# Performance work log

Hardware: AMD Instinct MI355X
Metric: run time of the kernel (lower is better)

Reference implementation:

```python
import jax, jax.numpy as jnp
import numpy as np

DIM = 512  # module's self.dim, used for the softmax scale (note: NOT head dim)

def setup_inputs() -> dict:
    key = jax.random.key(0)
    kq, kk, kv = jax.random.split(key, 3)
    shape = (4, 8, 2048, 64)  # [B, H, S, Dh]
    q = jax.random.normal(kq, shape, dtype=jnp.float32)
    k = jax.random.normal(kk, shape, dtype=jnp.float32)
    v = jax.random.normal(kv, shape, dtype=jnp.float32)
    return {"q": q, "k": k, "v": v, "n": 2048}

def reference(q, k, v, n):
    # scores = q @ k^T, then divide by sqrt(dim) AFTER matmul (as in source)
    scores = jnp.einsum('bhqd,bhkd->bhqk', q, k)
    scale = jnp.sqrt(jnp.asarray(DIM, dtype=scores.dtype))
    p_attn = jax.nn.softmax(scores / scale, axis=-1)
    return jnp.einsum('bhqk,bhkd->bhqd', p_attn, v)
```

## Files before the change

kernel.cpp:

```cpp
#include <hip/hip_runtime.h>


using half8   = __attribute__((ext_vector_type(8))) _Float16;
using half4   = __attribute__((ext_vector_type(4))) _Float16;
using half2v  = __attribute__((ext_vector_type(2))) _Float16;
using f32x4   = __attribute__((ext_vector_type(4))) float;
using f32x16  = __attribute__((ext_vector_type(16))) float;
using int4v   = __attribute__((ext_vector_type(4))) int;
using ushort8 = __attribute__((ext_vector_type(8))) unsigned short;

static __device__ __forceinline__ half2v cvt_pk(float a, float b) {
    return __builtin_bit_cast(half2v, __builtin_amdgcn_cvt_pkrtz(a, b));
}
static __device__ __forceinline__ int cvt_pk_i(float a, float b) {
    return __builtin_bit_cast(int, __builtin_amdgcn_cvt_pkrtz(a, b));
}

#define SEQ   2048
#define DH    64
#define QB    128
#define KVB   64
#define NKVT  (SEQ / KVB)
#define NQB   (SEQ / QB)
#define NBH   32
#define TILE_IMG_BYTES 16384
#define WS_NEED ((size_t)NBH * NKVT * TILE_IMG_BYTES)
#define QSCALE (1.4426950408889634f / 22.627416997969522f)

#if __has_builtin(__builtin_amdgcn_exp2f)
#define EXP2F __builtin_amdgcn_exp2f
#else
#define EXP2F exp2f
#endif

#define GLOAD4(dst, ptr) \
    asm volatile("global_load_dwordx4 %0, %1, off" : "=v"(dst) : "v"(ptr) : "memory")

#define WAIT_VM0()                                            \
    do {                                                      \
        asm volatile("s_waitcnt vmcnt(0)" ::: "memory");      \
        __builtin_amdgcn_sched_barrier(0);                    \
    } while (0)

#define LDS_BARRIER()                                         \
    do {                                                      \
        asm volatile("s_waitcnt lgkmcnt(0)" ::: "memory");    \
        __builtin_amdgcn_s_barrier();                         \
    } while (0)

#define PLSWAP(a, b) \
    asm volatile("s_nop 1\n\tv_permlane32_swap_b32 %0, %1" : "+v"(a), "+v"(b))

#define MFMA32(A, B, C) __builtin_amdgcn_mfma_f32_32x32x16_f16((A), (B), (C), 0, 0, 0)

static __device__ __forceinline__ f32x16 z16() {
    f32x16 v;
#pragma unroll
    for (int i = 0; i < 16; ++i) v[i] = 0.f;
    return v;
}

__global__ __launch_bounds__(256)
void prep_kv(const float* __restrict__ Kg, const float* __restrict__ Vg,
             char* __restrict__ ws)
{
    __shared__ unsigned short VT[64][72];
    const int bid = blockIdx.x;
    if (bid < 4096) {
        int id   = bid * 256 + threadIdx.x;
        int col4 = id & 15;
        int row  = (id >> 4) & 63;
        int kvt  = (id >> 10) & 31;
        int bh   = id >> 15;
        f32x4 v = *(const f32x4*)(Kg + ((size_t)(bh * SEQ) + kvt * 64 + row) * DH + col4 * 4);
        half2v lo = cvt_pk(v[0], v[1]);
        half2v hi = cvt_pk(v[2], v[3]);
        half4 h; h[0] = lo[0]; h[1] = lo[1]; h[2] = hi[0]; h[3] = hi[1];
        char* out = ws + (size_t)(bh * 32 + kvt) * TILE_IMG_BYTES
                       + ((row * 128 + col4 * 8) ^ ((row & 7) << 4));
        *(half4*)out = h;
    } else {
        int tb  = bid - 4096;
        int bh  = tb >> 5;
        int kvt = tb & 31;
        int tid = threadIdx.x;

        const float* vg = Vg + (size_t)(bh * SEQ) * DH + (size_t)(kvt * 64) * DH;
#pragma unroll
        for (int rr = 0; rr < 4; ++rr) {
            int kv = rr * 16 + (tid >> 4);
            int d4 = (tid & 15) * 4;
            f32x4 v = *(const f32x4*)(vg + (size_t)kv * DH + d4);
#pragma unroll
            for (int j = 0; j < 4; ++j)
                VT[d4 + j][kv] = __builtin_bit_cast(unsigned short, (_Float16)v[j]);
        }
        __syncthreads();

        int d   = tid >> 2;
        int seg = tid & 3;
        ushort8 h0, h1;
#pragma unroll
        for (int j = 0; j < 16; ++j) {
            int off = seg * 32 + j * 2;
            int kv  = (off ^ ((d & 7) << 4)) >> 1;
            unsigned short val = VT[d][kv];
            if (j < 8) h0[j] = val; else h1[j - 8] = val;
        }
        char* out = ws + (size_t)(bh * 32 + kvt) * TILE_IMG_BYTES + 8192 + d * 128 + seg * 32;
        *(ushort8*)(out)      = h0;
        *(ushort8*)(out + 16) = h1;
    }
}

__global__ __launch_bounds__(256, 2)
void fattn_fwd(const float* __restrict__ Qg, const char* __restrict__ Wimg,
               float* __restrict__ Og)
{
    __shared__ __align__(16) char KVl[2][TILE_IMG_BYTES];

    const int tid  = threadIdx.x;
    const int lane = tid & 63;
    const int wave = tid >> 6;
    const int l31  = lane & 31;
    const int hi   = lane >> 5;

    const int wg  = blockIdx.x;
    const int swz = (wg & 7) * 64 + (wg >> 3);
    const int qb  = swz & (NQB - 1);
    const int bh  = swz >> 4;
    const size_t base = (size_t)bh * (SEQ * DH);

    half8 qfrag[4];
    {
        const int qrow = qb * QB + wave * 32 + l31;
        const float* qp = Qg + base + (size_t)qrow * DH + hi * 8;
#pragma unroll
        for (int ks = 0; ks < 4; ++ks) {
            f32x4 a = *(const f32x4*)(qp + ks * 16);
            f32x4 b = *(const f32x4*)(qp + ks * 16 + 4);
            half8 f;
#pragma unroll
            for (int i = 0; i < 4; ++i) f[i]     = (_Float16)(a[i] * QSCALE);
#pragma unroll
            for (int i = 0; i < 4; ++i) f[i + 4] = (_Float16)(b[i] * QSCALE);
            qfrag[ks] = f;
        }
    }

    f32x16 acc0 = z16(), acc1 = z16();
    float lsum = 0.f;

    const char* imgbase = Wimg + (size_t)(bh * NKVT) * TILE_IMG_BYTES;
    f32x4 kreg[4];

    auto load_tile = [&](int kvt) {
        const char* img = imgbase + (size_t)kvt * TILE_IMG_BYTES;
#pragma unroll
        for (int it = 0; it < 4; ++it)
            GLOAD4(kreg[it], img + it * 4096 + tid * 16);
    };
    auto write_tile = [&](int b) {
        char* dst = KVl[b];
#pragma unroll
        for (int it = 0; it < 4; ++it)
            *(f32x4*)(dst + it * 4096 + tid * 16) = kreg[it];
    };

    load_tile(0);
    WAIT_VM0();
    write_tile(0);

    for (int kvt = 0; kvt < NKVT; ++kvt) {
        const int cur = kvt & 1;
        const char* kb = KVl[cur];
        const char* vb = KVl[cur] + 8192;

        if (kvt + 1 < NKVT) load_tile(kvt + 1);

        LDS_BARRIER();

        half8 kf[2][4];
#pragma unroll
        for (int kvs2 = 0; kvs2 < 2; ++kvs2)
#pragma unroll
            for (int ks = 0; ks < 4; ++ks) {
                int row  = kvs2 * 32 + l31;
                int byte = (row * 128 + ks * 32 + hi * 16) ^ ((row & 7) << 4);
                kf[kvs2][ks] = *(const half8*)(kb + byte);
            }
        f32x16 st0 = z16(), st1 = z16();
        __builtin_amdgcn_s_setprio(1);
#pragma unroll
        for (int ks = 0; ks < 4; ++ks) st0 = MFMA32(kf[0][ks], qfrag[ks], st0);
#pragma unroll
        for (int ks = 0; ks < 4; ++ks) st1 = MFMA32(kf[1][ks], qfrag[ks], st1);
        __builtin_amdgcn_s_setprio(0);

        half8 PA[4];
#pragma unroll
        for (int kvs2 = 0; kvs2 < 2; ++kvs2) {
            const f32x16& st = kvs2 ? st1 : st0;
            float p[16];
#pragma unroll
            for (int r = 0; r < 16; ++r) p[r] = EXP2F(st[r]);
            float s0 = 0.f, s1 = 0.f;
#pragma unroll
            for (int r = 0; r < 8; ++r) { s0 += p[r]; s1 += p[r + 8]; }
            lsum += s0 + s1;
            int m0 = cvt_pk_i(p[0],  p[1]),  m1 = cvt_pk_i(p[2],  p[3]);
            int m2 = cvt_pk_i(p[4],  p[5]),  m3 = cvt_pk_i(p[6],  p[7]);
            int m4 = cvt_pk_i(p[8],  p[9]),  m5 = cvt_pk_i(p[10], p[11]);
            int m6 = cvt_pk_i(p[12], p[13]), m7 = cvt_pk_i(p[14], p[15]);
            PLSWAP(m0, m2);
            PLSWAP(m1, m3);
            PLSWAP(m4, m6);
            PLSWAP(m5, m7);
            int4v t0; t0[0] = m0; t0[1] = m1; t0[2] = m2; t0[3] = m3;
            int4v t1; t1[0] = m4; t1[1] = m5; t1[2] = m6; t1[3] = m7;
            PA[2 * kvs2 + 0] = __builtin_bit_cast(half8, t0);
            PA[2 * kvs2 + 1] = __builtin_bit_cast(half8, t1);
        }

        half8 vf[2][4];
#pragma unroll
        for (int ds2 = 0; ds2 < 2; ++ds2)
#pragma unroll
            for (int ks = 0; ks < 4; ++ks) {
                int row  = ds2 * 32 + l31;
                int byte = (row * 128 + ks * 32 + hi * 16) ^ ((row & 7) << 4);
                vf[ds2][ks] = *(const half8*)(vb + byte);
            }
        __builtin_amdgcn_s_setprio(1);
#pragma unroll
        for (int ks = 0; ks < 4; ++ks) acc0 = MFMA32(PA[ks], vf[0][ks], acc0);
#pragma unroll
        for (int ks = 0; ks < 4; ++ks) acc1 = MFMA32(PA[ks], vf[1][ks], acc1);
        __builtin_amdgcn_s_setprio(0);

        if (kvt + 1 < NKVT) {
            WAIT_VM0();
            write_tile(cur ^ 1);
        }
    }

    lsum += __shfl_xor(lsum, 32);
    const float invl = 1.f / lsum;
    const int qstrip = qb * QB + wave * 32;
#pragma unroll
    for (int r = 0; r < 16; ++r) {
        int q16 = (r & 3) + 8 * (r >> 2) + 4 * hi;
        float sc = __shfl(invl, q16);
        float* op = Og + base + (size_t)(qstrip + q16) * DH;
        op[l31]      = acc0[r] * sc;
        op[32 + l31] = acc1[r] * sc;
    }
}

extern "C" void kernel_launch(void* const* d_in, const int* in_sizes, int n_in,
                              void* d_out, int out_size, void* d_ws, size_t ws_size,
                              hipStream_t stream) {
    const float* q = (const float*)d_in[0];
    const float* k = (const float*)d_in[1];
    const float* v = (const float*)d_in[2];
    float* o = (float*)d_out;
    char* ws = (char*)d_ws;
    prep_kv<<<dim3(5120, 1, 1), dim3(256, 1, 1), 0, stream>>>(k, v, ws);
    fattn_fwd<<<dim3(NQB * NBH, 1, 1), dim3(256, 1, 1), 0, stream>>>(q, ws, o);
}
```

Measured before the change: 64.58 us.

## Process two KV tiles per iteration with 4-slot LDS and interleaved MFMAs

The main loop now handles pairs of KV tiles. It loads 32KB per pair into a 4-buffer LDS ring and interleaves four independent QK^T MFMA chains, so each iteration needs half as many barriers and has more independent matrix work. The next pair's global loads are issued after the softmax rather than at the top of the loop. The costs are doubled LDS use (64KB per block), which may hurt the 2-blocks-per-CU target, more VGPRs for the 8 staging registers and the duplicated fragments, and a shorter window for hiding load latency.

```diff
diff --git a/kernel.cpp b/kernel.cpp
--- a/kernel.cpp
+++ b/kernel.cpp
@@ -21,10 +21,10 @@
 #define QB    128
 #define KVB   64
 #define NKVT  (SEQ / KVB)
+#define NITER (NKVT / 2)
 #define NQB   (SEQ / QB)
 #define NBH   32
 #define TILE_IMG_BYTES 16384
-#define WS_NEED ((size_t)NBH * NKVT * TILE_IMG_BYTES)
 #define QSCALE (1.4426950408889634f / 22.627416997969522f)
 
 #if __has_builtin(__builtin_amdgcn_exp2f)
@@ -48,6 +48,12 @@
         __builtin_amdgcn_s_barrier();                         \
     } while (0)
 
+#define LGKM_FENCE()                                          \
+    do {                                                      \
+        asm volatile("s_waitcnt lgkmcnt(0)" ::: "memory");    \
+        __builtin_amdgcn_sched_barrier(0);                    \
+    } while (0)
+
 #define PLSWAP(a, b) \
     asm volatile("s_nop 1\n\tv_permlane32_swap_b32 %0, %1" : "+v"(a), "+v"(b))
 
@@ -59,6 +65,31 @@
     for (int i = 0; i < 16; ++i) v[i] = 0.f;
     return v;
 }
+
+#define SOFTPACK(ST0, ST1, PA)                                            \
+    do {                                                                  \
+        _Pragma("unroll")                                                 \
+        for (int kvs2 = 0; kvs2 < 2; ++kvs2) {                            \
+            const f32x16& st_ = kvs2 ? (ST1) : (ST0);                     \
+            float p[16];                                                  \
+            _Pragma("unroll")                                             \
+            for (int r = 0; r < 16; ++r) p[r] = EXP2F(st_[r]);            \
+            float s0 = 0.f, s1 = 0.f;                                     \
+            _Pragma("unroll")                                             \
+            for (int r = 0; r < 8; ++r) { s0 += p[r]; s1 += p[r + 8]; }   \
+            lsum += s0 + s1;                                              \
+            int m0 = cvt_pk_i(p[0],  p[1]),  m1 = cvt_pk_i(p[2],  p[3]);  \
+            int m2 = cvt_pk_i(p[4],  p[5]),  m3 = cvt_pk_i(p[6],  p[7]);  \
+            int m4 = cvt_pk_i(p[8],  p[9]),  m5 = cvt_pk_i(p[10], p[11]); \
+            int m6 = cvt_pk_i(p[12], p[13]), m7 = cvt_pk_i(p[14], p[15]); \
+            PLSWAP(m0, m2); PLSWAP(m1, m3);                               \
+            PLSWAP(m4, m6); PLSWAP(m5, m7);                               \
+            int4v t0; t0[0] = m0; t0[1] = m1; t0[2] = m2; t0[3] = m3;     \
+            int4v t1; t1[0] = m4; t1[1] = m5; t1[2] = m6; t1[3] = m7;     \
+            (PA)[2 * kvs2 + 0] = __builtin_bit_cast(half8, t0);           \
+            (PA)[2 * kvs2 + 1] = __builtin_bit_cast(half8, t1);           \
+        }                                                                 \
+    } while (0)
 
 __global__ __launch_bounds__(256)
 void prep_kv(const float* __restrict__ Kg, const float* __restrict__ Vg,
@@ -117,7 +148,7 @@
 void fattn_fwd(const float* __restrict__ Qg, const char* __restrict__ Wimg,
                float* __restrict__ Og)
 {
-    __shared__ __align__(16) char KVl[2][TILE_IMG_BYTES];
+    __shared__ __align__(16) char KVl[4][TILE_IMG_BYTES];
 
     const int tid  = threadIdx.x;
     const int lane = tid & 63;
@@ -152,95 +183,97 @@
     float lsum = 0.f;
 
     const char* imgbase = Wimg + (size_t)(bh * NKVT) * TILE_IMG_BYTES;
-    f32x4 kreg[4];
-
-    auto load_tile = [&](int kvt) {
-        const char* img = imgbase + (size_t)kvt * TILE_IMG_BYTES;
-#pragma unroll
-        for (int it = 0; it < 4; ++it)
-            GLOAD4(kreg[it], img + it * 4096 + tid * 16);
+    f32x4 kreg[8];
+
+    auto load_pair = [&](int itp) {
+        const char* img = imgbase + (size_t)(2 * itp) * TILE_IMG_BYTES;
+#pragma unroll
+        for (int j = 0; j < 8; ++j)
+            GLOAD4(kreg[j], img + j * 4096 + tid * 16);
     };
-    auto write_tile = [&](int b) {
-        char* dst = KVl[b];
-#pragma unroll
-        for (int it = 0; it < 4; ++it)
-            *(f32x4*)(dst + it * 4096 + tid * 16) = kreg[it];
+    auto write_pair = [&](int p) {
+        char* dst = KVl[2 * p];
+#pragma unroll
+        for (int j = 0; j < 8; ++j)
+            *(f32x4*)(dst + j * 4096 + tid * 16) = kreg[j];
     };
 
-    load_tile(0);
+    load_pair(0);
     WAIT_VM0();
-    write_tile(0);
-
-    for (int kvt = 0; kvt < NKVT; ++kvt) {
-        const int cur = kvt & 1;
-        const char* kb = KVl[cur];
-        const char* vb = KVl[cur] + 8192;
-
-        if (kvt + 1 < NKVT) load_tile(kvt + 1);
+    write_pair(0);
+
+    for (int it = 0; it < NITER; ++it) {
+        const int pair = it & 1;
+        const char* kbA = KVl[2 * pair];
+        const char* kbB = KVl[2 * pair + 1];
 
         LDS_BARRIER();
 
-        half8 kf[2][4];
+        half8 kfA[2][4], kfB[2][4];
 #pragma unroll
         for (int kvs2 = 0; kvs2 < 2; ++kvs2)
 #pragma unroll
             for (int ks = 0; ks < 4; ++ks) {
                 int row  = kvs2 * 32 + l31;
                 int byte = (row * 128 + ks * 32 + hi * 16) ^ ((row & 7) << 4);
-                kf[kvs2][ks] = *(const half8*)(kb + byte);
+                kfA[kvs2][ks] = *(const half8*)(kbA + byte);
+                kfB[kvs2][ks] = *(const half8*)(kbB + byte);
             }
-        f32x16 st0 = z16(), st1 = z16();
+        LGKM_FENCE();
+
+        f32x16 st0A = z16(), st1A = z16(), st0B = z16(), st1B = z16();
         __builtin_amdgcn_s_setprio(1);
 #pragma unroll
-        for (int ks = 0; ks < 4; ++ks) st0 = MFMA32(kf[0][ks], qfrag[ks], st0);
-#pragma unroll
-        for (int ks = 0; ks < 4; ++ks) st1 = MFMA32(kf[1][ks], qfrag[ks], st1);
+        for (int ks = 0; ks < 4; ++ks) {
+            st0A = MFMA32(kfA[0][ks], qfrag[ks], st0A);
+            st1A = MFMA32(kfA[1][ks], qfrag[ks], st1A);
+            st0B = MFMA32(kfB[0][ks], qfrag[ks], st0B);
+            st1B = MFMA32(kfB[1][ks], qfrag[ks], st1B);
+        }
         __builtin_amdgcn_s_setprio(0);
 
-        half8 PA[4];
-#pragma unroll
-        for (int kvs2 = 0; kvs2 < 2; ++kvs2) {
-            const f32x16& st = kvs2 ? st1 : st0;
-            float p[16];
-#pragma unroll
-            for (int r = 0; r < 16; ++r) p[r] = EXP2F(st[r]);
-            float s0 = 0.f, s1 = 0.f;
-#pragma unroll
-            for (int r = 0; r < 8; ++r) { s0 += p[r]; s1 += p[r + 8]; }
-            lsum += s0 + s1;
-            int m0 = cvt_pk_i(p[0],  p[1]),  m1 = cvt_pk_i(p[2],  p[3]);
-            int m2 = cvt_pk_i(p[4],  p[5]),  m3 = cvt_pk_i(p[6],  p[7]);
-            int m4 = cvt_pk_i(p[8],  p[9]),  m5 = cvt_pk_i(p[10], p[11]);
-            int m6 = cvt_pk_i(p[12], p[13]), m7 = cvt_pk_i(p[14], p[15]);
-            PLSWAP(m0, m2);
-            PLSWAP(m1, m3);
-            PLSWAP(m4, m6);
-            PLSWAP(m5, m7);
-            int4v t0; t0[0] = m0; t0[1] = m1; t0[2] = m2; t0[3] = m3;
-            int4v t1; t1[0] = m4; t1[1] = m5; t1[2] = m6; t1[3] = m7;
-            PA[2 * kvs2 + 0] = __builtin_bit_cast(half8, t0);
-            PA[2 * kvs2 + 1] = __builtin_bit_cast(half8, t1);
-        }
-
-        half8 vf[2][4];
+        half8 vfA[2][4];
 #pragma unroll
         for (int ds2 = 0; ds2 < 2; ++ds2)
 #pragma unroll
             for (int ks = 0; ks < 4; ++ks) {
                 int row  = ds2 * 32 + l31;
                 int byte = (row * 128 + ks * 32 + hi * 16) ^ ((row & 7) << 4);
-                vf[ds2][ks] = *(const half8*)(vb + byte);
+                vfA[ds2][ks] = *(const half8*)(kbA + 8192 + byte);
             }
+        half8 PA_A[4];
+        SOFTPACK(st0A, st1A, PA_A);
+
+        half8 vfB[2][4];
+#pragma unroll
+        for (int ds2 = 0; ds2 < 2; ++ds2)
+#pragma unroll
+            for (int ks = 0; ks < 4; ++ks) {
+                int row  = ds2 * 32 + l31;
+                int byte = (row * 128 + ks * 32 + hi * 16) ^ ((row & 7) << 4);
+                vfB[ds2][ks] = *(const half8*)(kbB + 8192 + byte);
+            }
+        half8 PA_B[4];
+        SOFTPACK(st0B, st1B, PA_B);
+
+        if (it + 1 < NITER) load_pair(it + 1);
+
+        LGKM_FENCE();
+
         __builtin_amdgcn_s_setprio(1);
 #pragma unroll
-        for (int ks = 0; ks < 4; ++ks) acc0 = MFMA32(PA[ks], vf[0][ks], acc0);
-#pragma unroll
-        for (int ks = 0; ks < 4; ++ks) acc1 = MFMA32(PA[ks], vf[1][ks], acc1);
+        for (int ks = 0; ks < 4; ++ks) acc0 = MFMA32(PA_A[ks], vfA[0][ks], acc0);
+#pragma unroll
+        for (int ks = 0; ks < 4; ++ks) acc1 = MFMA32(PA_A[ks], vfA[1][ks], acc1);
+#pragma unroll
+        for (int ks = 0; ks < 4; ++ks) acc0 = MFMA32(PA_B[ks], vfB[0][ks], acc0);
+#pragma unroll
+        for (int ks = 0; ks < 4; ++ks) acc1 = MFMA32(PA_B[ks], vfB[1][ks], acc1);
         __builtin_amdgcn_s_setprio(0);
 
-        if (kvt + 1 < NKVT) {
+        if (it + 1 < NITER) {
             WAIT_VM0();
-            write_tile(cur ^ 1);
+            write_pair(pair ^ 1);
         }
     }
 
```

Result: slower. 65.90 us (+2.0%).
